# Performance work log

Hardware: AMD Instinct MI355X
Metric: run time of the kernel (lower is better)

Reference implementation:

```python
import jax, jax.numpy as jnp
import numpy as np

VOCAB = 50000
EMB = 256
HID = 256
MAX_PRED = 30
B = 64
S_ENC = 100


def setup_inputs() -> dict:
    key = jax.random.key(0)
    ks = jax.random.split(key, 16)
    s = 1.0 / np.sqrt(HID)
    return {
        "comment": jax.random.randint(ks[0], (B, 29), 0, VOCAB),
        "comment_input": jax.random.randint(ks[1], (B, 30), 0, VOCAB),
        "tok_output": jax.random.normal(ks[2], (B, S_ENC, HID), jnp.float32),
        "tok_enc_hc": jax.random.normal(ks[3], (1, B, HID), jnp.float32),
        "sbtao_output": jax.random.normal(ks[4], (B, S_ENC, HID), jnp.float32),
        "wemb": jax.random.normal(ks[5], (VOCAB, EMB), jnp.float32) * 0.02,
        "W_ih": jax.random.uniform(ks[6], (3 * HID, EMB), jnp.float32, -s, s),
        "W_hh": jax.random.uniform(ks[7], (3 * HID, HID), jnp.float32, -s, s),
        "b_ih": jax.random.uniform(ks[8], (3 * HID,), jnp.float32, -s, s),
        "b_hh": jax.random.uniform(ks[9], (3 * HID,), jnp.float32, -s, s),
        "W1": jax.random.uniform(ks[10], (HID, 3 * HID), jnp.float32, -s, s),
        "b1": jax.random.uniform(ks[11], (HID,), jnp.float32, -s, s),
        "W2": jax.random.uniform(ks[12], (VOCAB, HID), jnp.float32, -s, s),
        "b2": jax.random.uniform(ks[13], (VOCAB,), jnp.float32, -s, s),
    }


def _decode(comment_input, T, tok_output, h0, sbtao_output,
            wemb, W_ih, W_hh, b_ih, b_hh, W1, b1, W2, b2):
    # h0: [B,H]. The torch code re-uses hidden=tok_enc_hc at EVERY step,
    # so each step is an independent GRU-cell step -> vectorize over T.
    bsz = comment_input.shape[0]
    H = h0.shape[-1]
    emb = wemb[comment_input[:, :T]]                      # [B,T,E]
    gi = emb @ W_ih.T + b_ih                              # [B,T,3H]
    gh = h0 @ W_hh.T + b_hh                               # [B,3H]
    gh = gh[:, None, :]                                   # broadcast over T
    r = jax.nn.sigmoid(gi[..., :H] + gh[..., :H])
    z = jax.nn.sigmoid(gi[..., H:2 * H] + gh[..., H:2 * H])
    n = jnp.tanh(gi[..., 2 * H:] + r * gh[..., 2 * H:])
    dec = (1.0 - z) * n + z * h0[:, None, :]              # [B,T,H]

    def attend(enc):  # enc: [B,S,H]
        S = enc.shape[1]
        # Faithful to torch: keys come from a RESHAPE [B,S,H] -> [B,H,S]
        # (memory reinterpretation), not a transpose.
        keys = enc.reshape(bsz, H, S)
        a = jax.nn.softmax(jnp.einsum('bth,bhs->bts', dec, keys), axis=-1)
        return jnp.einsum('bts,bsh->bth', a, enc)         # [B,T,H]

    ctx = attend(tok_output)
    ast_ctx = attend(sbtao_output)
    cat = jnp.concatenate([ctx, dec, ast_ctx], axis=-1)   # [B,T,3H]
    out = jax.nn.relu(cat @ W1.T + b1)                    # [B,T,H]
    out = jax.nn.relu(out @ W2.T + b2)                    # [B,T,V]
    logprobs = jax.nn.log_softmax(out, axis=-1)           # [B,T,V]
    return logprobs


def reference(comment, comment_input, tok_output, tok_enc_hc, sbtao_output,
              wemb, W_ih, W_hh, b_ih, b_hh, W1, b1, W2, b2):
    T = min(comment.shape[1] + 1, MAX_PRED)
    h0 = tok_enc_hc[0]
    logprobs = _decode(comment_input, T, tok_output, h0, sbtao_output,
                       wemb, W_ih, W_hh, b_ih, b_hh, W1, b1, W2, b2)
    seq = jnp.argmax(logprobs, axis=-1).astype(jnp.int64 if jax.config.jax_enable_x64 else jnp.int32)
    return seq, logprobs
```

## Files before the change

### kernel.cpp

```cpp
#include <hip/hip_runtime.h>
#include <hip/hip_bf16.h>
#include <math.h>

#define NROW 1920
#define VOCAB_ 50000
#define NPAD 50048
#define NBLK 391
#define LDBF 72
#define CAP 128

typedef __attribute__((ext_vector_type(8))) short short8;
typedef __attribute__((ext_vector_type(4))) float floatx4;

__device__ inline ushort f32_to_bf16_bits(float f) {
    union { float f; unsigned u; } v; v.f = f;
    unsigned u = v.u;
    u += 0x7fffu + ((u >> 16) & 1u);
    return (ushort)(u >> 16);
}

__global__ void gather_emb_kernel(const int* __restrict__ tokens,
                                  const float* __restrict__ wemb,
                                  float* __restrict__ emb) {
    int n = blockIdx.x;
    int e = threadIdx.x;
    int tok = tokens[n];
    emb[(size_t)n * 256 + e] = wemb[(size_t)tok * 256 + e];
}

template <bool RELU>
__global__ __launch_bounds__(256) void gemm_nt_kernel(
    const float* __restrict__ A, const float* __restrict__ Bm,
    const float* __restrict__ bias, float* __restrict__ C,
    int M, int N, int K) {
    __shared__ float As[32][68];
    __shared__ float Bs[32][68];

    const int tid = threadIdx.x;
    const int m0 = blockIdx.y * 64;
    const int n0 = blockIdx.x * 64;
    const int tx = tid & 15;
    const int ty = tid >> 4;
    const int lrow = tid >> 3;
    const int lcol = (tid & 7) * 4;

    float acc[4][4];
#pragma unroll
    for (int i = 0; i < 4; ++i)
#pragma unroll
        for (int j = 0; j < 4; ++j) acc[i][j] = 0.f;

    for (int k0 = 0; k0 < K; k0 += 32) {
#pragma unroll
        for (int half = 0; half < 2; ++half) {
            int m = lrow + half * 32;
            float4 av = *reinterpret_cast<const float4*>(
                A + (size_t)(m0 + m) * K + k0 + lcol);
            As[lcol + 0][m] = av.x; As[lcol + 1][m] = av.y;
            As[lcol + 2][m] = av.z; As[lcol + 3][m] = av.w;
            int n = lrow + half * 32;
            float4 bv = make_float4(0.f, 0.f, 0.f, 0.f);
            if (n0 + n < N)
                bv = *reinterpret_cast<const float4*>(
                    Bm + (size_t)(n0 + n) * K + k0 + lcol);
            Bs[lcol + 0][n] = bv.x; Bs[lcol + 1][n] = bv.y;
            Bs[lcol + 2][n] = bv.z; Bs[lcol + 3][n] = bv.w;
        }
        __syncthreads();
#pragma unroll
        for (int k = 0; k < 32; ++k) {
            float4 a4 = *reinterpret_cast<const float4*>(&As[k][ty * 4]);
            float4 b4 = *reinterpret_cast<const float4*>(&Bs[k][tx * 4]);
            float a[4] = {a4.x, a4.y, a4.z, a4.w};
            float b[4] = {b4.x, b4.y, b4.z, b4.w};
#pragma unroll
            for (int i = 0; i < 4; ++i)
#pragma unroll
                for (int j = 0; j < 4; ++j) acc[i][j] = fmaf(a[i], b[j], acc[i][j]);
        }
        __syncthreads();
    }
#pragma unroll
    for (int i = 0; i < 4; ++i) {
        int m = m0 + ty * 4 + i;
#pragma unroll
        for (int j = 0; j < 4; ++j) {
            int n = n0 + tx * 4 + j;
            if (n < N) {
                float v = acc[i][j] + bias[n];
                if (RELU) v = fmaxf(v, 0.f);
                C[(size_t)m * N + n] = v;
            }
        }
    }
}

__global__ void dec_kernel(const float* __restrict__ gi,
                           const float* __restrict__ gh,
                           const float* __restrict__ h0,
                           float* __restrict__ cat) {
    int n = blockIdx.x;
    int h = threadIdx.x;
    int b = n / 30;
    float gir = gi[(size_t)n * 768 + h];
    float giz = gi[(size_t)n * 768 + 256 + h];
    float gin = gi[(size_t)n * 768 + 512 + h];
    float ghr = gh[(size_t)b * 768 + h];
    float ghz = gh[(size_t)b * 768 + 256 + h];
    float ghn = gh[(size_t)b * 768 + 512 + h];
    float r = 1.f / (1.f + expf(-(gir + ghr)));
    float z = 1.f / (1.f + expf(-(giz + ghz)));
    float nn = tanhf(gin + r * ghn);
    float h0v = h0[(size_t)b * 256 + h];
    cat[(size_t)n * 768 + 256 + h] = (1.f - z) * nn + z * h0v;
}

__global__ __launch_bounds__(256) void attn_kernel(
    const float* __restrict__ enc, float* __restrict__ cat, int colbase) {
    __shared__ float decs[256];
    __shared__ float sc[100];
    __shared__ float red[2];

    int n = blockIdx.x;
    int b = n / 30;
    int tid = threadIdx.x;

    decs[tid] = cat[(size_t)n * 768 + 256 + tid];
    __syncthreads();
    const float* e = enc + (size_t)b * 25600;
    if (tid < 100) {
        float acc = 0.f;
        for (int h = 0; h < 256; ++h) acc = fmaf(decs[h], e[h * 100 + tid], acc);
        sc[tid] = acc;
    }
    __syncthreads();
    if (tid == 0) {
        float mx = sc[0];
        for (int s = 1; s < 100; ++s) mx = fmaxf(mx, sc[s]);
        red[0] = mx;
    }
    __syncthreads();
    if (tid < 100) sc[tid] = expf(sc[tid] - red[0]);
    __syncthreads();
    if (tid == 0) {
        float sum = 0.f;
        for (int s = 0; s < 100; ++s) sum += sc[s];
        red[1] = 1.f / sum;
    }
    __syncthreads();
    float inv = red[1];
    float acc = 0.f;
    for (int s = 0; s < 100; ++s) acc = fmaf(sc[s], e[s * 256 + tid], acc);
    cat[(size_t)n * 768 + colbase + tid] = acc * inv;
}

__global__ void conv_out1_kernel(const float* __restrict__ src, ushort* __restrict__ dst) {
    size_t i = (size_t)blockIdx.x * 256 + threadIdx.x;
    dst[i] = f32_to_bf16_bits(src[i]);
}

__global__ void conv_w2_kernel(const float* __restrict__ W2, ushort* __restrict__ Wb) {
    int row = blockIdx.x;
    int col = threadIdx.x;
    float v = (row < VOCAB_) ? W2[(size_t)row * 256 + col] : 0.f;
    Wb[(size_t)row * 256 + col] = f32_to_bf16_bits(v);
}

template <int MODE>
__global__ __launch_bounds__(256) void mfma_gemm_kernel(
    const ushort* __restrict__ Abf, const ushort* __restrict__ Bbf,
    const float* __restrict__ b2, float* __restrict__ C,
    float* __restrict__ pmax, float* __restrict__ psum,
    const float* __restrict__ row_max, const float* __restrict__ row_lse,
    int* __restrict__ cnt, int* __restrict__ cand) {
    __shared__ ushort As[128 * LDBF];
    __shared__ ushort Bs[128 * LDBF];
    __shared__ float pmL[128][2];
    __shared__ float psL[128][2];

    const int tid = threadIdx.x;
    const int m0 = blockIdx.x * 128;
    const int n0 = blockIdx.y * 128;
    const int nblk = blockIdx.y;
    const int wave = tid >> 6, lane = tid & 63;
    const int wm = wave >> 1, wn = wave & 1;
    const int q = lane >> 4, ln = lane & 15;

    const int srow = tid >> 1;
    const int sseg = (tid & 1) * 32;

    floatx4 acc[4][4];
#pragma unroll
    for (int i = 0; i < 4; ++i)
#pragma unroll
        for (int j = 0; j < 4; ++j) acc[i][j] = (floatx4)0.f;

    for (int k0 = 0; k0 < 256; k0 += 64) {
        const uint4* asrc = reinterpret_cast<const uint4*>(
            Abf + (size_t)(m0 + srow) * 256 + k0 + sseg);
        uint4 a0 = asrc[0], a1 = asrc[1], a2 = asrc[2], a3 = asrc[3];
        const uint4* bsrc = reinterpret_cast<const uint4*>(
            Bbf + (size_t)(n0 + srow) * 256 + k0 + sseg);
        uint4 c0 = bsrc[0], c1 = bsrc[1], c2 = bsrc[2], c3 = bsrc[3];
        __syncthreads();
        uint4* ad = reinterpret_cast<uint4*>(&As[srow * LDBF + sseg]);
        ad[0] = a0; ad[1] = a1; ad[2] = a2; ad[3] = a3;
        uint4* bd = reinterpret_cast<uint4*>(&Bs[srow * LDBF + sseg]);
        bd[0] = c0; bd[1] = c1; bd[2] = c2; bd[3] = c3;
        __syncthreads();
#pragma unroll
        for (int ks = 0; ks < 2; ++ks) {
            short8 af[4], bf[4];
#pragma unroll
            for (int mt = 0; mt < 4; ++mt)
                af[mt] = *reinterpret_cast<const short8*>(
                    &As[(wm * 64 + mt * 16 + ln) * LDBF + ks * 32 + q * 8]);
#pragma unroll
            for (int nt = 0; nt < 4; ++nt)
                bf[nt] = *reinterpret_cast<const short8*>(
                    &Bs[(wn * 64 + nt * 16 + ln) * LDBF + ks * 32 + q * 8]);
#pragma unroll
            for (int mt = 0; mt < 4; ++mt)
#pragma unroll
                for (int nt = 0; nt < 4; ++nt)
                    acc[mt][nt] = __builtin_amdgcn_mfma_f32_16x16x32_bf16(
                        af[mt], bf[nt], acc[mt][nt], 0, 0, 0);
        }
    }

    float bias[4]; int nn[4];
#pragma unroll
    for (int nt = 0; nt < 4; ++nt) {
        int n = n0 + wn * 64 + nt * 16 + ln;
        nn[nt] = n;
        bias[nt] = (n < VOCAB_) ? b2[n] : 0.f;
    }

    if (MODE == 0) {
#pragma unroll
        for (int mt = 0; mt < 4; ++mt) {
#pragma unroll
            for (int r = 0; r < 4; ++r) {
                float vv[4]; float lmax = -1e30f;
#pragma unroll
                for (int nt = 0; nt < 4; ++nt) {
                    float v = acc[mt][nt][r] + bias[nt];
                    v = fmaxf(v, 0.f);
                    if (nn[nt] >= VOCAB_) v = -1e30f;
                    vv[nt] = v;
                    lmax = fmaxf(lmax, v);
                }
#pragma unroll
                for (int off = 1; off < 16; off <<= 1)
                    lmax = fmaxf(lmax, __shfl_xor(lmax, off, 64));
                float ls = 0.f;
#pragma unroll
                for (int nt = 0; nt < 4; ++nt) ls += __expf(vv[nt] - lmax);
#pragma unroll
                for (int off = 1; off < 16; off <<= 1)
                    ls += __shfl_xor(ls, off, 64);
                if (ln == 0) {
                    int rl = wm * 64 + mt * 16 + q * 4 + r;
                    pmL[rl][wn] = lmax;
                    psL[rl][wn] = ls;
                }
            }
        }
        __syncthreads();
        if (tid < 128) {
            float m1 = pmL[tid][0], m2 = pmL[tid][1];
            float nm = fmaxf(m1, m2);
            float s = psL[tid][0] * __expf(m1 - nm) + psL[tid][1] * __expf(m2 - nm);
            pmax[(size_t)(m0 + tid) * NBLK + nblk] = nm;
            psum[(size_t)(m0 + tid) * NBLK + nblk] = s;
        }
    } else {
#pragma unroll
        for (int mt = 0; mt < 4; ++mt) {
#pragma unroll
            for (int r = 0; r < 4; ++r) {
                int m = m0 + wm * 64 + mt * 16 + q * 4 + r;
                float thr = row_max[m] - 0.03f;
                float rl = row_lse[m];
#pragma unroll
                for (int nt = 0; nt < 4; ++nt) {
                    if (nn[nt] < VOCAB_) {
                        float v = acc[mt][nt][r] + bias[nt];
                        v = fmaxf(v, 0.f);
                        C[(size_t)m * VOCAB_ + nn[nt]] = v - rl;
                        if (v >= thr) {
                            int k = atomicAdd(&cnt[m], 1);
                            if (k < CAP) cand[m * CAP + k] = nn[nt];
                        }
                    }
                }
            }
        }
    }
}

__global__ __launch_bounds__(128) void reduce_rows_kernel(
    const float* __restrict__ pmax, const float* __restrict__ psum,
    float* __restrict__ row_max, float* __restrict__ row_lse,
    int* __restrict__ cnt) {
    __shared__ float sm[128], ss[128];
    int row = blockIdx.x, tid = threadIdx.x;
    if (tid == 0) cnt[row] = 0;
    const float* pm = pmax + (size_t)row * NBLK;
    const float* ps = psum + (size_t)row * NBLK;
    float m = -1e30f, s = 0.f;
    for (int i = tid; i < NBLK; i += 128) {
        float m2 = pm[i], s2 = ps[i];
        float nm = fmaxf(m, m2);
        s = s * __expf(m - nm) + s2 * __expf(m2 - nm);
        m = nm;
    }
    sm[tid] = m; ss[tid] = s;
    __syncthreads();
    for (int off = 64; off > 0; off >>= 1) {
        if (tid < off) {
            float m2 = sm[tid + off], s2 = ss[tid + off];
            float nm = fmaxf(sm[tid], m2);
            ss[tid] = ss[tid] * __expf(sm[tid] - nm) + s2 * __expf(m2 - nm);
            sm[tid] = nm;
        }
        __syncthreads();
    }
    if (tid == 0) {
        row_max[row] = sm[0];
        row_lse[row] = sm[0] + logf(ss[0]);
    }
}

__global__ __launch_bounds__(256) void final_cand_kernel(
    const int* __restrict__ cnt, const int* __restrict__ cand,
    const float* __restrict__ out1, const float* __restrict__ W2,
    const float* __restrict__ b2, float* __restrict__ seq) {
    __shared__ float o1s[256];
    __shared__ double red[256];
    __shared__ double bestv_s;
    __shared__ int besti_s;

    int row = blockIdx.x, tid = threadIdx.x;
    if (tid == 0) { bestv_s = -1e300; besti_s = 0x7fffffff; }
    o1s[tid] = out1[(size_t)row * 256 + tid];
    __syncthreads();

    int nc = min(cnt[row], CAP);
    for (int j = 0; j < nc; ++j) {
        int c = cand[row * CAP + j];
        red[tid] = (double)o1s[tid] * (double)W2[(size_t)c * 256 + tid];
        __syncthreads();
        for (int off = 128; off > 0; off >>= 1) {
            if (tid < off) red[tid] += red[tid + off];
            __syncthreads();
        }
        if (tid == 0) {
            double v = red[0] + (double)b2[c];
            if (v < 0.0) v = 0.0;
            if (v > bestv_s || (v == bestv_s && c < besti_s)) { bestv_s = v; besti_s = c; }
        }
        __syncthreads();
    }
    if (tid == 0) seq[row] = (float)(besti_s == 0x7fffffff ? 0 : besti_s);
}

extern "C" void kernel_launch(void* const* d_in, const int* in_sizes, int n_in,
                              void* d_out, int out_size, void* d_ws, size_t ws_size,
                              hipStream_t stream) {
    const int* comment_input = (const int*)d_in[1];
    const float* tok_output  = (const float*)d_in[2];
    const float* h0          = (const float*)d_in[3];
    const float* sbtao       = (const float*)d_in[4];
    const float* wemb        = (const float*)d_in[5];
    const float* W_ih        = (const float*)d_in[6];
    const float* W_hh        = (const float*)d_in[7];
    const float* b_ih        = (const float*)d_in[8];
    const float* b_hh        = (const float*)d_in[9];
    const float* W1          = (const float*)d_in[10];
    const float* b1          = (const float*)d_in[11];
    const float* W2          = (const float*)d_in[12];
    const float* b2          = (const float*)d_in[13];

    float* out    = (float*)d_out;
    float* seq    = out;
    float* logits = out + NROW;

    float* ws      = (float*)d_ws;
    float* emb     = ws;
    float* gi      = emb + 491520;
    float* gh      = gi + 1474560;
    float* cat     = gh + 49152;
    float* out1    = cat + 1474560;
    float* pmax    = out1 + 491520;
    float* psum    = pmax + 750720;
    float* row_max = psum + 750720;
    float* row_lse = row_max + 1920;
    ushort* out1b  = (ushort*)(row_lse + 1920);
    ushort* W2b    = (ushort*)(row_lse + 1920 + 245760);
    int* cnt       = (int*)emb;
    int* cand      = cnt + 1920;

    gather_emb_kernel<<<NROW, 256, 0, stream>>>(comment_input, wemb, emb);

    gemm_nt_kernel<false><<<dim3(12, 1), 256, 0, stream>>>(
        h0, W_hh, b_hh, gh, 64, 768, 256);
    gemm_nt_kernel<false><<<dim3(12, 30), 256, 0, stream>>>(
        emb, W_ih, b_ih, gi, NROW, 768, 256);
    dec_kernel<<<NROW, 256, 0, stream>>>(gi, gh, h0, cat);
    attn_kernel<<<NROW, 256, 0, stream>>>(tok_output, cat, 0);
    attn_kernel<<<NROW, 256, 0, stream>>>(sbtao, cat, 512);
    gemm_nt_kernel<true><<<dim3(4, 30), 256, 0, stream>>>(
        cat, W1, b1, out1, NROW, 256, 768);

    conv_out1_kernel<<<NROW, 256, 0, stream>>>(out1, out1b);
    conv_w2_kernel<<<NPAD, 256, 0, stream>>>(W2, W2b);

    mfma_gemm_kernel<0><<<dim3(15, NBLK), 256, 0, stream>>>(
        out1b, W2b, b2, logits, pmax, psum, nullptr, nullptr, nullptr, nullptr);

    reduce_rows_kernel<<<NROW, 128, 0, stream>>>(pmax, psum, row_max, row_lse, cnt);

    mfma_gemm_kernel<1><<<dim3(15, NBLK), 256, 0, stream>>>(
        out1b, W2b, b2, logits, nullptr, nullptr, row_max, row_lse, cnt, cand);

    final_cand_kernel<<<NROW, 256, 0, stream>>>(
        cnt, cand, out1, W2, b2, seq);
}
```

Before: 867.4 us.

## Use direct global-to-LDS loads in MFMA GEMM and fuse out1 bf16 conversion

The MFMA vocab GEMM now stages A and B tiles with global_load_lds (16-byte direct-to-LDS loads), replacing register staging. Because those loads write each row contiguously, the LDS padding is dropped and the row stride becomes 64. The conversion of out1 to bf16 moves into the W1 GEMM epilogue, which removes one kernel launch and one pass over out1. The unpadded 128-byte stride can cause LDS bank conflicts on the fragment reads, and the GEMM stays single-buffered with no overlap between loads and compute.

```diff
diff --git a/kernel.cpp b/kernel.cpp
--- a/kernel.cpp
+++ b/kernel.cpp
@@ -6,7 +6,6 @@
 #define VOCAB_ 50000
 #define NPAD 50048
 #define NBLK 391
-#define LDBF 72
 #define CAP 128
 
 typedef __attribute__((ext_vector_type(8))) short short8;
@@ -32,6 +31,7 @@
 __global__ __launch_bounds__(256) void gemm_nt_kernel(
     const float* __restrict__ A, const float* __restrict__ Bm,
     const float* __restrict__ bias, float* __restrict__ C,
+    ushort* __restrict__ Cbf,
     int M, int N, int K) {
     __shared__ float As[32][68];
     __shared__ float Bs[32][68];
@@ -90,6 +90,7 @@
                 float v = acc[i][j] + bias[n];
                 if (RELU) v = fmaxf(v, 0.f);
                 C[(size_t)m * N + n] = v;
+                if (Cbf) Cbf[(size_t)m * N + n] = f32_to_bf16_bits(v);
             }
         }
     }
@@ -154,11 +155,6 @@
     cat[(size_t)n * 768 + colbase + tid] = acc * inv;
 }
 
-__global__ void conv_out1_kernel(const float* __restrict__ src, ushort* __restrict__ dst) {
-    size_t i = (size_t)blockIdx.x * 256 + threadIdx.x;
-    dst[i] = f32_to_bf16_bits(src[i]);
-}
-
 __global__ void conv_w2_kernel(const float* __restrict__ W2, ushort* __restrict__ Wb) {
     int row = blockIdx.x;
     int col = threadIdx.x;
@@ -173,8 +169,8 @@
     float* __restrict__ pmax, float* __restrict__ psum,
     const float* __restrict__ row_max, const float* __restrict__ row_lse,
     int* __restrict__ cnt, int* __restrict__ cand) {
-    __shared__ ushort As[128 * LDBF];
-    __shared__ ushort Bs[128 * LDBF];
+    __shared__ ushort As[128 * 64];
+    __shared__ ushort Bs[128 * 64];
     __shared__ float pmL[128][2];
     __shared__ float psL[128][2];
 
@@ -186,8 +182,8 @@
     const int wm = wave >> 1, wn = wave & 1;
     const int q = lane >> 4, ln = lane & 15;
 
-    const int srow = tid >> 1;
-    const int sseg = (tid & 1) * 32;
+    const int lrow = lane >> 3;
+    const int lcol8 = (lane & 7) * 8;
 
     floatx4 acc[4][4];
 #pragma unroll
@@ -196,17 +192,21 @@
         for (int j = 0; j < 4; ++j) acc[i][j] = (floatx4)0.f;
 
     for (int k0 = 0; k0 < 256; k0 += 64) {
-        const uint4* asrc = reinterpret_cast<const uint4*>(
-            Abf + (size_t)(m0 + srow) * 256 + k0 + sseg);
-        uint4 a0 = asrc[0], a1 = asrc[1], a2 = asrc[2], a3 = asrc[3];
-        const uint4* bsrc = reinterpret_cast<const uint4*>(
-            Bbf + (size_t)(n0 + srow) * 256 + k0 + sseg);
-        uint4 c0 = bsrc[0], c1 = bsrc[1], c2 = bsrc[2], c3 = bsrc[3];
-        __syncthreads();
-        uint4* ad = reinterpret_cast<uint4*>(&As[srow * LDBF + sseg]);
-        ad[0] = a0; ad[1] = a1; ad[2] = a2; ad[3] = a3;
-        uint4* bd = reinterpret_cast<uint4*>(&Bs[srow * LDBF + sseg]);
-        bd[0] = c0; bd[1] = c1; bd[2] = c2; bd[3] = c3;
+        __syncthreads();
+#pragma unroll
+        for (int c = 0; c < 4; ++c) {
+            int rbase = wave * 32 + c * 8;
+            const ushort* ga = Abf + (size_t)(m0 + rbase + lrow) * 256 + k0 + lcol8;
+            const ushort* gb = Bbf + (size_t)(n0 + rbase + lrow) * 256 + k0 + lcol8;
+            __builtin_amdgcn_global_load_lds(
+                (const __attribute__((address_space(1))) unsigned int*)ga,
+                (__attribute__((address_space(3))) unsigned int*)&As[rbase * 64],
+                16, 0, 0);
+            __builtin_amdgcn_global_load_lds(
+                (const __attribute__((address_space(1))) unsigned int*)gb,
+                (__attribute__((address_space(3))) unsigned int*)&Bs[rbase * 64],
+                16, 0, 0);
+        }
         __syncthreads();
 #pragma unroll
         for (int ks = 0; ks < 2; ++ks) {
@@ -214,11 +214,11 @@
 #pragma unroll
             for (int mt = 0; mt < 4; ++mt)
                 af[mt] = *reinterpret_cast<const short8*>(
-                    &As[(wm * 64 + mt * 16 + ln) * LDBF + ks * 32 + q * 8]);
+                    &As[(wm * 64 + mt * 16 + ln) * 64 + ks * 32 + q * 8]);
 #pragma unroll
             for (int nt = 0; nt < 4; ++nt)
                 bf[nt] = *reinterpret_cast<const short8*>(
-                    &Bs[(wn * 64 + nt * 16 + ln) * LDBF + ks * 32 + q * 8]);
+                    &Bs[(wn * 64 + nt * 16 + ln) * 64 + ks * 32 + q * 8]);
 #pragma unroll
             for (int mt = 0; mt < 4; ++mt)
 #pragma unroll
@@ -404,16 +404,15 @@
     gather_emb_kernel<<<NROW, 256, 0, stream>>>(comment_input, wemb, emb);
 
     gemm_nt_kernel<false><<<dim3(12, 1), 256, 0, stream>>>(
-        h0, W_hh, b_hh, gh, 64, 768, 256);
+        h0, W_hh, b_hh, gh, nullptr, 64, 768, 256);
     gemm_nt_kernel<false><<<dim3(12, 30), 256, 0, stream>>>(
-        emb, W_ih, b_ih, gi, NROW, 768, 256);
+        emb, W_ih, b_ih, gi, nullptr, NROW, 768, 256);
     dec_kernel<<<NROW, 256, 0, stream>>>(gi, gh, h0, cat);
     attn_kernel<<<NROW, 256, 0, stream>>>(tok_output, cat, 0);
     attn_kernel<<<NROW, 256, 0, stream>>>(sbtao, cat, 512);
     gemm_nt_kernel<true><<<dim3(4, 30), 256, 0, stream>>>(
-        cat, W1, b1, out1, NROW, 256, 768);
-
-    conv_out1_kernel<<<NROW, 256, 0, stream>>>(out1, out1b);
+        cat, W1, b1, out1, out1b, NROW, 256, 768);
+
     conv_w2_kernel<<<NPAD, 256, 0, stream>>>(W2, W2b);
 
     mfma_gemm_kernel<0><<<dim3(15, NBLK), 256, 0, stream>>>(
```

After: 873.9 us. Within noise of the previous version (+0.8%).
